# Kernel tuning notes

Hardware: AMD Instinct MI355X
Metric: run time of the kernel (lower is better)

Reference implementation:

```python
import jax, jax.numpy as jnp
import numpy as np

BATCH = 16384
D_INPUT = 2048
HIDDEN = 256
N_CLASSES = 1000
N_STEPS = 25
BETA = 0.9
THRESHOLD = 1.0


def setup_inputs() -> dict:
    key = jax.random.key(0)
    kx, k1, k2, k3, k4 = jax.random.split(key, 5)
    x = jax.random.normal(kx, (BATCH, D_INPUT), dtype=jnp.float32)
    W1 = jax.random.normal(k1, (HIDDEN, D_INPUT), dtype=jnp.float32) * 0.02
    b1 = jax.random.normal(k2, (HIDDEN,), dtype=jnp.float32) * 0.02
    W2 = jax.random.normal(k3, (N_CLASSES, HIDDEN), dtype=jnp.float32) * 0.02
    b2 = jax.random.normal(k4, (N_CLASSES,), dtype=jnp.float32) * 0.02
    return {"x": x, "W1": W1, "b1": b1, "W2": W2, "b2": b2}


def reference(x, W1, b1, W2, b2):
    batch = x.shape[0]
    # fc1(x) is identical every step (x does not change); compute once.
    cur1 = jnp.einsum('bd,hd->bh', x, W1) + b1  # [B, HIDDEN]

    def step(carry, _):
        mem1, mem2, spike_count = carry
        mem1 = BETA * mem1 + cur1
        spk1 = jax.nn.sigmoid(10.0 * (mem1 - THRESHOLD))
        mem1 = mem1 * (1.0 - spk1)
        cur2 = jnp.einsum('bh,ch->bc', spk1, W2) + b2  # [B, N_CLASSES]
        mem2 = BETA * mem2 + cur2
        spk2 = jax.nn.sigmoid(10.0 * (mem2 - THRESHOLD))
        mem2 = mem2 * (1.0 - spk2)
        return (mem1, mem2, spike_count + spk2), spk1

    init = (
        jnp.zeros((batch, HIDDEN), dtype=x.dtype),
        jnp.zeros((batch, N_CLASSES), dtype=x.dtype),
        jnp.zeros((batch, N_CLASSES), dtype=x.dtype),
    )
    (mem1, mem2, spike_count), spk1_all = jax.lax.scan(step, init, None, length=N_STEPS)
    sparsity = spk1_all[-1].mean()  # mean of last-step spk1, as in original
    return spike_count / N_STEPS, sparsity
```

## Files before the change

### kernel.cpp

```cpp
#include <hip/hip_runtime.h>
#include <cstdint>
#include <cstddef>

typedef __attribute__((ext_vector_type(4))) float    f32x4;
typedef __attribute__((ext_vector_type(4))) float    float4v;
typedef __attribute__((ext_vector_type(8))) _Float16 half8;
typedef __attribute__((ext_vector_type(4))) _Float16 half4;

#define BATCH   16384
#define DIN     2048
#define HID     256
#define NCLS    1000
#define NCLSP   1024
#define NSTEPS  25
#define BETA    0.9f
#define SGK     14.4269504089f
#define SCL     4096.0f
#define ISCL    (1.0f/4096.0f)

#define WS_CUR1   0
#define WS_W2H    16777216
#define WS_W2L    17301504
#define WS_B2P    17825792
#define WS_SPARS  17829888

__device__ __forceinline__ float sigmoid10(float m) {
  float z = __builtin_fmaf(-SGK, m, SGK);
  float e = __builtin_amdgcn_exp2f(z);
  return __builtin_amdgcn_rcpf(1.0f + e);
}

__global__ void k_cast_w2(const float* __restrict__ W2, const float* __restrict__ b2,
                          _Float16* __restrict__ W2h, _Float16* __restrict__ W2l,
                          float* __restrict__ b2p) {
  int row = blockIdx.x;
  int t   = threadIdx.x;
  float v = (row < NCLS) ? W2[(size_t)row * HID + t] : 0.0f;
  _Float16 h = (_Float16)v;
  _Float16 l = (_Float16)((v - (float)h) * SCL);
  W2h[(size_t)row * HID + t] = h;
  W2l[(size_t)row * HID + t] = l;
  if (t == 0) b2p[row] = (row < NCLS) ? b2[row] : 0.0f;
}

#define ROWB1 144
__global__ __launch_bounds__(512) void k_fc1(
    const float* __restrict__ x, const float* __restrict__ W1,
    const float* __restrict__ b1, float* __restrict__ cur1) {
  extern __shared__ char smem[];
  char* xh = smem;
  char* xl = smem + 9216;
  char* wh = smem + 18432;
  char* wl = smem + 55296;
  const int tid = threadIdx.x;
  const int l   = tid & 63;
  const int w   = tid >> 6;
  const int wm  = w >> 2;
  const int wn  = w & 3;
  const int l15 = l & 15, lq = l >> 4;
  const int mbase = blockIdx.x * 64;

  f32x4 am[2][4], ac[2][4];
#pragma unroll
  for (int i = 0; i < 2; ++i)
#pragma unroll
    for (int j = 0; j < 4; ++j) { am[i][j] = f32x4{0,0,0,0}; ac[i][j] = f32x4{0,0,0,0}; }

  const int srow = tid >> 4;
  const int c4   = (tid & 15) * 4;

#pragma unroll 1
  for (int kt = 0; kt < DIN / 64; ++kt) {
    const int k0 = kt * 64;
#pragma unroll
    for (int j = 0; j < 2; ++j) {
      int r = j * 32 + srow;
      float4v v = *(const float4v*)(x + (size_t)(mbase + r) * DIN + k0 + c4);
      half4 h, lo;
#pragma unroll
      for (int e = 0; e < 4; ++e) {
        _Float16 hv = (_Float16)v[e];
        h[e]  = hv;
        lo[e] = (_Float16)((v[e] - (float)hv) * SCL);
      }
      *(half4*)(xh + r * ROWB1 + (tid & 15) * 8) = h;
      *(half4*)(xl + r * ROWB1 + (tid & 15) * 8) = lo;
    }
#pragma unroll
    for (int j = 0; j < 8; ++j) {
      int r = j * 32 + srow;
      float4v v = *(const float4v*)(W1 + (size_t)r * DIN + k0 + c4);
      half4 h, lo;
#pragma unroll
      for (int e = 0; e < 4; ++e) {
        _Float16 hv = (_Float16)v[e];
        h[e]  = hv;
        lo[e] = (_Float16)((v[e] - (float)hv) * SCL);
      }
      *(half4*)(wh + r * ROWB1 + (tid & 15) * 8) = h;
      *(half4*)(wl + r * ROWB1 + (tid & 15) * 8) = lo;
    }
    __syncthreads();
#pragma unroll
    for (int fk = 0; fk < 2; ++fk) {
      const int g16 = (fk * 4 + lq) * 16;
      half8 ah[2], al[2], bh[4], bl[4];
#pragma unroll
      for (int fm = 0; fm < 2; ++fm) {
        int r = wm * 32 + fm * 16 + l15;
        ah[fm] = *(const half8*)(xh + r * ROWB1 + g16);
        al[fm] = *(const half8*)(xl + r * ROWB1 + g16);
      }
#pragma unroll
      for (int fn = 0; fn < 4; ++fn) {
        int r = wn * 64 + fn * 16 + l15;
        bh[fn] = *(const half8*)(wh + r * ROWB1 + g16);
        bl[fn] = *(const half8*)(wl + r * ROWB1 + g16);
      }
#pragma unroll
      for (int fm = 0; fm < 2; ++fm)
#pragma unroll
        for (int fn = 0; fn < 4; ++fn) {
          am[fm][fn] = __builtin_amdgcn_mfma_f32_16x16x32_f16(ah[fm], bh[fn], am[fm][fn], 0, 0, 0);
          ac[fm][fn] = __builtin_amdgcn_mfma_f32_16x16x32_f16(ah[fm], bl[fn], ac[fm][fn], 0, 0, 0);
          ac[fm][fn] = __builtin_amdgcn_mfma_f32_16x16x32_f16(al[fm], bh[fn], ac[fm][fn], 0, 0, 0);
        }
    }
    __syncthreads();
  }
#pragma unroll
  for (int fn = 0; fn < 4; ++fn) {
    int h = wn * 64 + fn * 16 + l15;
    float b1v = b1[h];
#pragma unroll
    for (int fm = 0; fm < 2; ++fm) {
      int m0 = mbase + wm * 32 + fm * 16 + lq * 4;
#pragma unroll
      for (int e = 0; e < 4; ++e)
        cur1[(size_t)(m0 + e) * HID + h] = am[fm][fn][e] + ac[fm][fn][e] * ISCL + b1v;
    }
  }
}

#define ROWH 528
__global__ __launch_bounds__(512) void k_fc2d(
    const float* __restrict__ cur1, const _Float16* __restrict__ W2h,
    const _Float16* __restrict__ W2l, const float* __restrict__ b2p,
    float* __restrict__ outp, float* __restrict__ spars) {
  extern __shared__ char smem[];
  char* Ah = smem;
  char* Al = smem + 32 * ROWH;
  const int tid = threadIdx.x;
  const int l   = tid & 63;
  const int w   = tid >> 6;
  const int l15 = l & 15, lq = l >> 4;
  const int ct  = blockIdx.x;
  const int mt  = blockIdx.y;
  const int mb  = mt * 32;
  const int cls = ct * 128 + w * 16 + l15;

  half8 whf[8], wlf[8];
#pragma unroll
  for (int fk = 0; fk < 8; ++fk) {
    whf[fk] = *(const half8*)(W2h + (size_t)cls * HID + (fk * 4 + lq) * 8);
    wlf[fk] = *(const half8*)(W2l + (size_t)cls * HID + (fk * 4 + lq) * 8);
  }
  const float b2v = b2p[cls];

  const int r0 = tid >> 4;
  const int h0 = (tid & 15) * 16;
  f32x4 cr[4], m1[4];
#pragma unroll
  for (int j = 0; j < 4; ++j) {
    cr[j] = *(const float4v*)(cur1 + (size_t)(mb + r0) * HID + h0 + j * 4);
    m1[j] = f32x4{0,0,0,0};
  }

  f32x4 mem2[2], cnt[2];
#pragma unroll
  for (int fm = 0; fm < 2; ++fm) { mem2[fm] = f32x4{0,0,0,0}; cnt[fm] = f32x4{0,0,0,0}; }

  float ssum = 0.0f;

#pragma unroll 1
  for (int t = 0; t < NSTEPS; ++t) {
    half8 sh[2], sl[2];
#pragma unroll
    for (int j = 0; j < 4; ++j) {
      m1[j] = m1[j] * BETA + cr[j];
#pragma unroll
      for (int e = 0; e < 4; ++e) {
        float s = sigmoid10(m1[j][e]);
        m1[j][e] = __builtin_fmaf(-s, m1[j][e], m1[j][e]);
        _Float16 hv = (_Float16)s;
        sh[j >> 1][(j & 1) * 4 + e] = hv;
        sl[j >> 1][(j & 1) * 4 + e] = (_Float16)((s - (float)hv) * SCL);
        if (t == NSTEPS - 1) ssum += s;
      }
    }
    *(half8*)(Ah + r0 * ROWH + h0 * 2)      = sh[0];
    *(half8*)(Ah + r0 * ROWH + h0 * 2 + 16) = sh[1];
    *(half8*)(Al + r0 * ROWH + h0 * 2)      = sl[0];
    *(half8*)(Al + r0 * ROWH + h0 * 2 + 16) = sl[1];
    __syncthreads();

    f32x4 am2[2], ac2[2];
#pragma unroll
    for (int fm = 0; fm < 2; ++fm) {
      am2[fm] = mem2[fm] * BETA + b2v;
      ac2[fm] = f32x4{0,0,0,0};
    }
#pragma unroll
    for (int fk = 0; fk < 8; ++fk) {
      const int g16 = (fk * 4 + lq) * 16;
      half8 ah[2], al[2];
#pragma unroll
      for (int fm = 0; fm < 2; ++fm) {
        int r = fm * 16 + l15;
        ah[fm] = *(const half8*)(Ah + r * ROWH + g16);
        al[fm] = *(const half8*)(Al + r * ROWH + g16);
      }
#pragma unroll
      for (int fm = 0; fm < 2; ++fm) {
        am2[fm] = __builtin_amdgcn_mfma_f32_16x16x32_f16(ah[fm], whf[fk], am2[fm], 0, 0, 0);
        ac2[fm] = __builtin_amdgcn_mfma_f32_16x16x32_f16(ah[fm], wlf[fk], ac2[fm], 0, 0, 0);
        ac2[fm] = __builtin_amdgcn_mfma_f32_16x16x32_f16(al[fm], whf[fk], ac2[fm], 0, 0, 0);
      }
    }
#pragma unroll
    for (int fm = 0; fm < 2; ++fm) {
#pragma unroll
      for (int e = 0; e < 4; ++e) {
        float c2 = am2[fm][e] + ac2[fm][e] * ISCL;
        float s2 = sigmoid10(c2);
        mem2[fm][e] = __builtin_fmaf(-s2, c2, c2);
        cnt[fm][e] += s2;
      }
    }
    __syncthreads();
  }

#pragma unroll
  for (int fm = 0; fm < 2; ++fm) {
    if (cls < NCLS) {
      int m0 = mb + fm * 16 + lq * 4;
#pragma unroll
      for (int e = 0; e < 4; ++e)
        outp[(size_t)(m0 + e) * NCLS + cls] = cnt[fm][e] * (1.0f / NSTEPS);
    }
  }
  if (ct == 0) {
#pragma unroll
    for (int off = 32; off; off >>= 1) ssum += __shfl_down(ssum, off, 64);
    if (l == 0) atomicAdd(spars, ssum);
  }
}

__global__ void k_fin(const float* __restrict__ spars, float* __restrict__ outp) {
  if (threadIdx.x == 0 && blockIdx.x == 0)
    outp[(size_t)BATCH * NCLS] = spars[0] * (1.0f / ((float)BATCH * (float)HID));
}

extern "C" void kernel_launch(void* const* d_in, const int* in_sizes, int n_in,
                              void* d_out, int out_size, void* d_ws, size_t ws_size,
                              hipStream_t stream) {
  const float* x  = (const float*)d_in[0];
  const float* W1 = (const float*)d_in[1];
  const float* b1 = (const float*)d_in[2];
  const float* W2 = (const float*)d_in[3];
  const float* b2 = (const float*)d_in[4];
  float* outp = (float*)d_out;
  char* ws = (char*)d_ws;

  float*    cur1 = (float*)(ws + WS_CUR1);
  _Float16* W2h  = (_Float16*)(ws + WS_W2H);
  _Float16* W2l  = (_Float16*)(ws + WS_W2L);
  float*    b2p  = (float*)(ws + WS_B2P);
  float*    spars= (float*)(ws + WS_SPARS);

  (void)in_sizes; (void)n_in; (void)out_size; (void)ws_size;

  static bool attr_set = false;
  if (!attr_set) {
    hipFuncSetAttribute((const void*)k_fc1,
                        hipFuncAttributeMaxDynamicSharedMemorySize, 92160);
    attr_set = true;
  }

  hipMemsetAsync(spars, 0, sizeof(float), stream);
  k_cast_w2<<<dim3(NCLSP), dim3(HID), 0, stream>>>(W2, b2, W2h, W2l, b2p);
  k_fc1<<<dim3(BATCH / 64), dim3(512), 92160, stream>>>(x, W1, b1, cur1);
  k_fc2d<<<dim3(NCLSP / 128, BATCH / 32), dim3(512), 33792, stream>>>(cur1, W2h, W2l, b2p, outp, spars);
  k_fin<<<dim3(1), dim3(64), 0, stream>>>(spars, outp);
}
```

Measured before the change: 1.224 ms.

## Restructure fc2 recurrence with 32x32 MFMA, double-buffered spikes and LDS state

The fused fc2 kernel now gives each block 256 classes and uses 32x32x16 MFMA tiles, so each wave holds twice as many W2 fragments in registers. Spike tiles are double-buffered in LDS with an XOR-style swizzle, which lets the next step's layer-1 update run while the current step's MFMAs consume the other buffer, and removes one barrier per step. cur1 and the spike counts move into LDS to free registers. The cost is a much larger LDS allocation (about 137 KB per block), which limits occupancy, and a heavier register load from the 16-wide accumulators.

```diff
diff --git a/kernel.cpp b/kernel.cpp
--- a/kernel.cpp
+++ b/kernel.cpp
@@ -2,10 +2,12 @@
 #include <cstdint>
 #include <cstddef>
 
-typedef __attribute__((ext_vector_type(4))) float    f32x4;
-typedef __attribute__((ext_vector_type(4))) float    float4v;
-typedef __attribute__((ext_vector_type(8))) _Float16 half8;
-typedef __attribute__((ext_vector_type(4))) _Float16 half4;
+typedef __attribute__((ext_vector_type(4)))  float    f32x4;
+typedef __attribute__((ext_vector_type(16))) float    f32x16;
+typedef __attribute__((ext_vector_type(4)))  float    float4v;
+typedef __attribute__((ext_vector_type(8)))  _Float16 f16x8;
+typedef __attribute__((ext_vector_type(4)))  _Float16 half4;
+typedef __attribute__((ext_vector_type(8)))  _Float16 half8;
 
 #define BATCH   16384
 #define DIN     2048
@@ -142,52 +144,63 @@
   }
 }
 
-#define ROWH 528
-__global__ __launch_bounds__(512) void k_fc2d(
+#define LDS_CR   65536
+#define LDS_CNT  98816
+#define LDS_TOT  139776
+__global__ __launch_bounds__(512, 2) void k_fc2d(
     const float* __restrict__ cur1, const _Float16* __restrict__ W2h,
     const _Float16* __restrict__ W2l, const float* __restrict__ b2p,
     float* __restrict__ outp, float* __restrict__ spars) {
   extern __shared__ char smem[];
-  char* Ah = smem;
-  char* Al = smem + 32 * ROWH;
+  char* crb  = smem + LDS_CR;
+  char* cntb = smem + LDS_CNT;
   const int tid = threadIdx.x;
   const int l   = tid & 63;
   const int w   = tid >> 6;
-  const int l15 = l & 15, lq = l >> 4;
+  const int l31 = l & 31;
+  const int hi  = l >> 5;
   const int ct  = blockIdx.x;
   const int mt  = blockIdx.y;
   const int mb  = mt * 32;
-  const int cls = ct * 128 + w * 16 + l15;
-
-  half8 whf[8], wlf[8];
-#pragma unroll
-  for (int fk = 0; fk < 8; ++fk) {
-    whf[fk] = *(const half8*)(W2h + (size_t)cls * HID + (fk * 4 + lq) * 8);
-    wlf[fk] = *(const half8*)(W2l + (size_t)cls * HID + (fk * 4 + lq) * 8);
+  const int cls = ct * 256 + w * 32 + l31;
+
+  f16x8 whf[16], wlf[16];
+#pragma unroll
+  for (int k = 0; k < 16; ++k) {
+    size_t o = (size_t)cls * HID + k * 16 + hi * 8;
+    whf[k] = *(const f16x8*)(W2h + o);
+    wlf[k] = *(const f16x8*)(W2l + o);
   }
   const float b2v = b2p[cls];
 
-  const int r0 = tid >> 4;
-  const int h0 = (tid & 15) * 16;
-  f32x4 cr[4], m1[4];
+  const int r0  = tid >> 4;
+  const int c15 = tid & 15;
+  const int h0  = c15 * 16;
+
+  f32x4 cr0[4];
 #pragma unroll
   for (int j = 0; j < 4; ++j) {
-    cr[j] = *(const float4v*)(cur1 + (size_t)(mb + r0) * HID + h0 + j * 4);
-    m1[j] = f32x4{0,0,0,0};
-  }
-
-  f32x4 mem2[2], cnt[2];
-#pragma unroll
-  for (int fm = 0; fm < 2; ++fm) { mem2[fm] = f32x4{0,0,0,0}; cnt[fm] = f32x4{0,0,0,0}; }
-
+    cr0[j] = *(const float4v*)(cur1 + (size_t)(mb + r0) * HID + h0 + j * 4);
+    *(f32x4*)(crb + r0 * 1040 + c15 * 64 + j * 16) = cr0[j];
+  }
+#pragma unroll
+  for (int j = 0; j < 4; ++j)
+    *(f32x4*)(cntb + tid * 80 + j * 16) = f32x4{0,0,0,0};
+
+  const int cb  = c15 * 2;
+  const int wb0 = r0 * 512 + (((cb     + 2 * r0) & 31) << 4);
+  const int wb1 = r0 * 512 + (((cb + 1 + 2 * r0) & 31) << 4);
+
+  f32x4 m1[4];
+#pragma unroll
+  for (int j = 0; j < 4; ++j) m1[j] = f32x4{0,0,0,0};
   float ssum = 0.0f;
 
-#pragma unroll 1
-  for (int t = 0; t < NSTEPS; ++t) {
-    half8 sh[2], sl[2];
+  {
+    f16x8 sh[2], sl[2];
 #pragma unroll
     for (int j = 0; j < 4; ++j) {
-      m1[j] = m1[j] * BETA + cr[j];
+      m1[j] = m1[j] * BETA + cr0[j];
 #pragma unroll
       for (int e = 0; e < 4; ++e) {
         float s = sigmoid10(m1[j][e]);
@@ -195,58 +208,88 @@
         _Float16 hv = (_Float16)s;
         sh[j >> 1][(j & 1) * 4 + e] = hv;
         sl[j >> 1][(j & 1) * 4 + e] = (_Float16)((s - (float)hv) * SCL);
-        if (t == NSTEPS - 1) ssum += s;
-      }
-    }
-    *(half8*)(Ah + r0 * ROWH + h0 * 2)      = sh[0];
-    *(half8*)(Ah + r0 * ROWH + h0 * 2 + 16) = sh[1];
-    *(half8*)(Al + r0 * ROWH + h0 * 2)      = sl[0];
-    *(half8*)(Al + r0 * ROWH + h0 * 2 + 16) = sl[1];
+      }
+    }
+    *(f16x8*)(smem + wb0)         = sh[0];
+    *(f16x8*)(smem + wb1)         = sh[1];
+    *(f16x8*)(smem + 16384 + wb0) = sl[0];
+    *(f16x8*)(smem + 16384 + wb1) = sl[1];
+  }
+  __syncthreads();
+
+  f32x16 mem2;
+#pragma unroll
+  for (int e = 0; e < 16; ++e) mem2[e] = 0.0f;
+
+  const int arow = l31 * 512;
+
+#pragma unroll 1
+  for (int t = 0; t < NSTEPS; ++t) {
+    char* bufc = smem + ((t & 1) << 15);
+    char* bufn = smem + (((t + 1) & 1) << 15);
+
+    f32x16 am, ac;
+#pragma unroll
+    for (int e = 0; e < 16; ++e) { am[e] = __builtin_fmaf(BETA, mem2[e], b2v); ac[e] = 0.0f; }
+
+#pragma unroll
+    for (int k = 0; k < 16; ++k) {
+      int ad = arow + (((2 * k + hi + 2 * l31) & 31) << 4);
+      f16x8 ah = *(const f16x8*)(bufc + ad);
+      f16x8 al = *(const f16x8*)(bufc + 16384 + ad);
+      am = __builtin_amdgcn_mfma_f32_32x32x16_f16(ah, whf[k], am, 0, 0, 0);
+      ac = __builtin_amdgcn_mfma_f32_32x32x16_f16(ah, wlf[k], ac, 0, 0, 0);
+      ac = __builtin_amdgcn_mfma_f32_32x32x16_f16(al, whf[k], ac, 0, 0, 0);
+    }
+
+    if (t < NSTEPS - 1) {
+      f16x8 sh[2], sl[2];
+#pragma unroll
+      for (int j = 0; j < 4; ++j) {
+        f32x4 c = *(const f32x4*)(crb + r0 * 1040 + c15 * 64 + j * 16);
+        m1[j] = m1[j] * BETA + c;
+#pragma unroll
+        for (int e = 0; e < 4; ++e) {
+          float s = sigmoid10(m1[j][e]);
+          m1[j][e] = __builtin_fmaf(-s, m1[j][e], m1[j][e]);
+          _Float16 hv = (_Float16)s;
+          sh[j >> 1][(j & 1) * 4 + e] = hv;
+          sl[j >> 1][(j & 1) * 4 + e] = (_Float16)((s - (float)hv) * SCL);
+          if (t + 1 == NSTEPS - 1) ssum += s;
+        }
+      }
+      *(f16x8*)(bufn + wb0)         = sh[0];
+      *(f16x8*)(bufn + wb1)         = sh[1];
+      *(f16x8*)(bufn + 16384 + wb0) = sl[0];
+      *(f16x8*)(bufn + 16384 + wb1) = sl[1];
+    }
+
+#pragma unroll
+    for (int j = 0; j < 4; ++j) {
+      f32x4 cn = *(const f32x4*)(cntb + tid * 80 + j * 16);
+#pragma unroll
+      for (int e = 0; e < 4; ++e) {
+        int q = j * 4 + e;
+        float c2 = __builtin_fmaf(ac[q], ISCL, am[q]);
+        float s2 = sigmoid10(c2);
+        mem2[q] = __builtin_fmaf(-s2, c2, c2);
+        cn[e] += s2;
+      }
+      *(f32x4*)(cntb + tid * 80 + j * 16) = cn;
+    }
     __syncthreads();
-
-    f32x4 am2[2], ac2[2];
-#pragma unroll
-    for (int fm = 0; fm < 2; ++fm) {
-      am2[fm] = mem2[fm] * BETA + b2v;
-      ac2[fm] = f32x4{0,0,0,0};
-    }
-#pragma unroll
-    for (int fk = 0; fk < 8; ++fk) {
-      const int g16 = (fk * 4 + lq) * 16;
-      half8 ah[2], al[2];
-#pragma unroll
-      for (int fm = 0; fm < 2; ++fm) {
-        int r = fm * 16 + l15;
-        ah[fm] = *(const half8*)(Ah + r * ROWH + g16);
-        al[fm] = *(const half8*)(Al + r * ROWH + g16);
-      }
-#pragma unroll
-      for (int fm = 0; fm < 2; ++fm) {
-        am2[fm] = __builtin_amdgcn_mfma_f32_16x16x32_f16(ah[fm], whf[fk], am2[fm], 0, 0, 0);
-        ac2[fm] = __builtin_amdgcn_mfma_f32_16x16x32_f16(ah[fm], wlf[fk], ac2[fm], 0, 0, 0);
-        ac2[fm] = __builtin_amdgcn_mfma_f32_16x16x32_f16(al[fm], whf[fk], ac2[fm], 0, 0, 0);
-      }
-    }
-#pragma unroll
-    for (int fm = 0; fm < 2; ++fm) {
-#pragma unroll
-      for (int e = 0; e < 4; ++e) {
-        float c2 = am2[fm][e] + ac2[fm][e] * ISCL;
-        float s2 = sigmoid10(c2);
-        mem2[fm][e] = __builtin_fmaf(-s2, c2, c2);
-        cnt[fm][e] += s2;
-      }
-    }
-    __syncthreads();
-  }
-
-#pragma unroll
-  for (int fm = 0; fm < 2; ++fm) {
-    if (cls < NCLS) {
-      int m0 = mb + fm * 16 + lq * 4;
-#pragma unroll
-      for (int e = 0; e < 4; ++e)
-        outp[(size_t)(m0 + e) * NCLS + cls] = cnt[fm][e] * (1.0f / NSTEPS);
+  }
+
+  if (cls < NCLS) {
+#pragma unroll
+    for (int j = 0; j < 4; ++j) {
+      f32x4 cn = *(const f32x4*)(cntb + tid * 80 + j * 16);
+#pragma unroll
+      for (int e = 0; e < 4; ++e) {
+        int q = j * 4 + e;
+        int rloc = (q & 3) + 8 * (q >> 2) + 4 * hi;
+        outp[(size_t)(mb + rloc) * NCLS + cls] = cn[e] * (1.0f / NSTEPS);
+      }
     }
   }
   if (ct == 0) {
@@ -280,16 +323,14 @@
 
   (void)in_sizes; (void)n_in; (void)out_size; (void)ws_size;
 
-  static bool attr_set = false;
-  if (!attr_set) {
-    hipFuncSetAttribute((const void*)k_fc1,
-                        hipFuncAttributeMaxDynamicSharedMemorySize, 92160);
-    attr_set = true;
-  }
+  hipFuncSetAttribute((const void*)k_fc1,
+                      hipFuncAttributeMaxDynamicSharedMemorySize, 92160);
+  hipFuncSetAttribute((const void*)k_fc2d,
+                      hipFuncAttributeMaxDynamicSharedMemorySize, LDS_TOT);
 
   hipMemsetAsync(spars, 0, sizeof(float), stream);
   k_cast_w2<<<dim3(NCLSP), dim3(HID), 0, stream>>>(W2, b2, W2h, W2l, b2p);
   k_fc1<<<dim3(BATCH / 64), dim3(512), 92160, stream>>>(x, W1, b1, cur1);
-  k_fc2d<<<dim3(NCLSP / 128, BATCH / 32), dim3(512), 33792, stream>>>(cur1, W2h, W2l, b2p, outp, spars);
+  k_fc2d<<<dim3(NCLSP / 256, BATCH / 32), dim3(512), LDS_TOT, stream>>>(cur1, W2h, W2l, b2p, outp, spars);
   k_fin<<<dim3(1), dim3(64), 0, stream>>>(spars, outp);
 }
```

After: 1.082 ms. -11.5%, faster.
